# Kernel tuning notes

Measured on AMD Instinct MI355X. Metric: run time of the kernel, lower is better.

## Reference

```python
import jax, jax.numpy as jnp
import numpy as np

ALPHA = 0.5  # leaking rate, matches init_kwargs


def setup_inputs() -> dict:
    key = jax.random.key(0)
    k_x, k_i2h, k_h2h, k_ow, k_ob = jax.random.split(key, 5)
    B, T, I = 64, 256, 128
    R, O = 2048, 10
    x = jax.random.normal(k_x, (B, T, I), dtype=jnp.float32)
    # i2h_w ~ (1/sqrt(R)) * N(0,1), as in the torch module
    i2h_w = jax.random.normal(k_i2h, (I, R), dtype=jnp.float32) / np.sqrt(R)
    # h2h: random Gaussian rescaled so spectral radius ~ 0.9 (Gaussian NxN has
    # spectral radius ~ sqrt(N)); the torch code does the exact eig-based rescale
    # plus the leaky transform baked into h2h. We emulate the scale here.
    h2h = jax.random.normal(k_h2h, (R, R), dtype=jnp.float32) * (0.9 / np.sqrt(R))
    out_w = jax.random.normal(k_ow, (R, O), dtype=jnp.float32)
    out_b = jax.random.normal(k_ob, (O,), dtype=jnp.float32)
    return {"x": x, "i2h_w": i2h_w, "h2h": h2h, "out_w": out_w, "out_b": out_b}


def reference(x, i2h_w, h2h, out_w, out_b):
    # x: (B, T, I). Sequential leaky-ESN scan over T.
    B, T, I = x.shape
    R = h2h.shape[0]
    # Precompute input projections for all timesteps in one GEMM: (B, T, R)
    xin = jnp.einsum("bti,ir->btr", x, i2h_w)
    res0 = jnp.zeros((B, R), dtype=x.dtype)

    def step(res, xin_t):
        cand = jnp.tanh(xin_t + res @ h2h)
        res_new = (1.0 - ALPHA) * res + ALPHA * cand
        return res_new, res_new

    res_last, res_seq = jax.lax.scan(step, res0, jnp.swapaxes(xin, 0, 1))  # res_seq: (T, B, R)
    hiddens = jnp.swapaxes(res_seq, 0, 1)  # (B, T, R)
    # OUTPUT_TYPE.LAST_OUT -> readout of the final reservoir state
    out = res_last @ out_w + out_b  # (B, O)
    return out, hiddens
```

## Files before the change

### kernel.cpp

```cpp
#include <hip/hip_runtime.h>


typedef _Float16 f16x8 __attribute__((ext_vector_type(8)));
typedef float f32x4 __attribute__((ext_vector_type(4)));
typedef float f32x2 __attribute__((ext_vector_type(2)));

#define NB 64
#define RDIM 2048
#define TT 256
#define IDIM 128
#define NWG 128
#define NTHR 512


__global__ __launch_bounds__(256) void transpose_f32_to_f16(
    const float* __restrict__ in, _Float16* __restrict__ out, int rows, int cols) {
  __shared__ float tile[64][65];
  const int tx = threadIdx.x & 63;
  const int ty = threadIdx.x >> 6;
  const int rbase = blockIdx.y * 64;
  const int cbase = blockIdx.x * 64;
  for (int rr = ty; rr < 64; rr += 4)
    tile[rr][tx] = in[(size_t)(rbase + rr) * cols + cbase + tx];
  __syncthreads();
  for (int rr = ty; rr < 64; rr += 4)
    out[(size_t)(cbase + rr) * rows + rbase + tx] = (_Float16)tile[tx][rr];
}

__global__ __launch_bounds__(256) void convert_f32_f16(
    const float* __restrict__ in, _Float16* __restrict__ out, int n) {
  int i = blockIdx.x * 256 + threadIdx.x;
  int stride = gridDim.x * 256;
  for (; i < n; i += stride) out[i] = (_Float16)in[i];
}

__global__ __launch_bounds__(256) void init_zero(
    unsigned* __restrict__ res_words, unsigned* __restrict__ ctr_words) {
  int i = blockIdx.x * 256 + threadIdx.x;
  if (i < NB * RDIM / 2) res_words[i] = 0;
  if (i < 4096) ctr_words[i] = 0;
}


__device__ __forceinline__ f16x8 load_res16(const _Float16* p) {
  union { unsigned long long u[2]; f16x8 v; } r;
  const unsigned long long* q = (const unsigned long long*)p;
  r.u[0] = __hip_atomic_load(q, __ATOMIC_RELAXED, __HIP_MEMORY_SCOPE_SYSTEM);
  r.u[1] = __hip_atomic_load(q + 1, __ATOMIC_RELAXED, __HIP_MEMORY_SCOPE_SYSTEM);
  return r.v;
}

__device__ __forceinline__ void waitflag(const unsigned* p, unsigned tgt) {
  if (__hip_atomic_load(p, __ATOMIC_RELAXED, __HIP_MEMORY_SCOPE_SYSTEM) >= tgt) return;
  do {
    __builtin_amdgcn_s_sleep(1);
  } while (__hip_atomic_load(p, __ATOMIC_RELAXED, __HIP_MEMORY_SCOPE_SYSTEM) < tgt);
}

__device__ __forceinline__ float tanh_fast(float x) {
  float e = __expf(2.0f * x);
  return 1.0f - 2.0f * __builtin_amdgcn_rcpf(e + 1.0f);
}

__device__ __forceinline__ f32x4 MF(f16x8 a, f16x8 b, f32x4 c) {
  return __builtin_amdgcn_mfma_f32_16x16x32_f16(a, b, c, 0, 0, 0);
}


__global__ __launch_bounds__(NTHR, 2) void esn_persist(
    const _Float16* __restrict__ h2hT,
    const _Float16* __restrict__ i2hT,
    const _Float16* __restrict__ x16,
    _Float16* __restrict__ resbuf,
    float* __restrict__ pout,
    unsigned* __restrict__ ctrs,
    const float* __restrict__ out_w,
    const float* __restrict__ out_b,
    float* __restrict__ out)
{
  const int bid = blockIdx.x;
  const int rh = bid >> 6;
  const int g = bid & 63;
  const int jbase = g * 32;
  const int rbase = rh * 32;
  const int tid = threadIdx.x;
  const int wave = tid >> 6;
  const int lane = tid & 63;
  const int l15 = lane & 15;
  const int q = lane >> 4;
  const int kslice = wave * 256;

  f16x8 bfr[8][2];
#pragma unroll
  for (int kt = 0; kt < 8; ++kt)
#pragma unroll
    for (int nt = 0; nt < 2; ++nt) {
      int n_abs = jbase + nt * 16 + l15;
      bfr[kt][nt] = *(const f16x8*)(h2hT + (size_t)n_abs * RDIM + kslice + kt * 32 + q * 8);
    }
  f16x8 ib[2] = {};
  if (wave < 4) {
#pragma unroll
    for (int nt = 0; nt < 2; ++nt) {
      int n_abs = jbase + nt * 16 + l15;
      ib[nt] = *(const f16x8*)(i2hT + (size_t)n_abs * IDIM + wave * 32 + q * 8);
    }
  }

  const unsigned* fpoll = ctrs + 16 * (rh * 64 + wave * 8 + (lane & 7));

  __shared__ __align__(16) float pl[8][32][36];

  const int m = tid >> 4;
  const int c2 = (tid & 15) * 2;
  float s[2];
  s[0] = 0.f; s[1] = 0.f;

  for (int t = 0; t < TT; ++t) {
    const _Float16* resp = resbuf + (size_t)(t & 1) * (NB * RDIM);
    const unsigned tgt = (unsigned)t;

    f32x4 acc[2][2] = {};

    if (wave < 4) {
#pragma unroll
      for (int mt = 0; mt < 2; ++mt) {
        f16x8 ax = *(const f16x8*)(x16 + ((size_t)(rbase + mt * 16 + l15) * TT + t) * IDIM + wave * 32 + q * 8);
        acc[mt][0] = MF(ax, ib[0], acc[mt][0]);
        acc[mt][1] = MF(ax, ib[1], acc[mt][1]);
      }
    }

    {
      unsigned v = __hip_atomic_load(fpoll, __ATOMIC_RELAXED, __HIP_MEMORY_SCOPE_SYSTEM);
      while (!__all(v >= tgt)) {
        __builtin_amdgcn_s_sleep(1);
        v = __hip_atomic_load(fpoll, __ATOMIC_RELAXED, __HIP_MEMORY_SCOPE_SYSTEM);
      }
    }

    f16x8 A[8][2];
#pragma unroll
    for (int kt = 0; kt < 8; ++kt)
#pragma unroll
      for (int mt = 0; mt < 2; ++mt)
        A[kt][mt] = load_res16(resp + (size_t)(rbase + mt * 16 + l15) * RDIM + kslice + kt * 32 + q * 8);
#pragma unroll
    for (int kt = 0; kt < 8; ++kt)
#pragma unroll
      for (int mt = 0; mt < 2; ++mt) {
        acc[mt][0] = MF(A[kt][mt], bfr[kt][0], acc[mt][0]);
        acc[mt][1] = MF(A[kt][mt], bfr[kt][1], acc[mt][1]);
      }

#pragma unroll
    for (int mt = 0; mt < 2; ++mt)
#pragma unroll
      for (int nt = 0; nt < 2; ++nt)
#pragma unroll
        for (int r = 0; r < 4; ++r)
          pl[wave][mt * 16 + q * 4 + r][nt * 16 + l15] = acc[mt][nt][r];
    __syncthreads();

    f32x2 v = *(const f32x2*)&pl[0][m][c2];
#pragma unroll
    for (int w = 1; w < 8; ++w) v += *(const f32x2*)&pl[w][m][c2];

    union { _Float16 h[2]; unsigned u; } frag;
#pragma unroll
    for (int r = 0; r < 2; ++r) {
      s[r] = 0.5f * s[r] + 0.5f * tanh_fast(v[r]);
      frag.h[r] = (_Float16)s[r];
    }

    _Float16* resw = resbuf + (size_t)((t + 1) & 1) * (NB * RDIM);
    __hip_atomic_store((unsigned*)(resw + (size_t)(rbase + m) * RDIM + jbase + c2),
                       frag.u, __ATOMIC_RELAXED, __HIP_MEMORY_SCOPE_SYSTEM);
    __syncthreads();
    if (tid == 0)
      __hip_atomic_store(&ctrs[16 * bid], (unsigned)(t + 1), __ATOMIC_RELAXED,
                         __HIP_MEMORY_SCOPE_SYSTEM);

    f32x2 hv;
    hv[0] = s[0]; hv[1] = s[1];
    float* hid = out + 640 + ((size_t)(rbase + m) * TT + t) * RDIM + jbase + c2;
    __builtin_nontemporal_store(hv, (f32x2*)hid);
  }

  if (bid < 16) {
    if (tid == 0) {
      for (int rh2 = 0; rh2 < 2; ++rh2)
        for (int j = 0; j < 4; ++j)
          waitflag(ctrs + 16 * (rh2 * 64 + 4 * bid + j), (unsigned)TT);
    }
    __syncthreads();
    const _Float16* rlast = resbuf;
    for (int o = tid; o < 640; o += NTHR) {
      int b = o / 10, oo = o - 10 * b;
      float a = 0.f;
      const unsigned* rp = (const unsigned*)(rlast + (size_t)b * RDIM + bid * 128);
      for (int r2 = 0; r2 < 64; ++r2) {
        union { unsigned u; _Float16 h[2]; } cv;
        cv.u = __hip_atomic_load(rp + r2, __ATOMIC_RELAXED, __HIP_MEMORY_SCOPE_SYSTEM);
        a += (float)cv.h[0] * out_w[(size_t)(bid * 128 + 2 * r2) * 10 + oo];
        a += (float)cv.h[1] * out_w[(size_t)(bid * 128 + 2 * r2 + 1) * 10 + oo];
      }
      __hip_atomic_store(&pout[bid * 640 + o], a, __ATOMIC_RELAXED, __HIP_MEMORY_SCOPE_SYSTEM);
    }
    __syncthreads();
    if (tid == 0)
      __hip_atomic_fetch_add(&ctrs[2048], 1u, __ATOMIC_RELAXED, __HIP_MEMORY_SCOPE_SYSTEM);
    if (bid == 0) {
      if (tid == 0) {
        while (__hip_atomic_load(&ctrs[2048], __ATOMIC_RELAXED, __HIP_MEMORY_SCOPE_SYSTEM) < 16u)
          __builtin_amdgcn_s_sleep(1);
      }
      __syncthreads();
      for (int o = tid; o < 640; o += NTHR) {
        float a = out_b[o % 10];
        for (int kk = 0; kk < 16; ++kk)
          a += __hip_atomic_load(&pout[kk * 640 + o], __ATOMIC_RELAXED, __HIP_MEMORY_SCOPE_SYSTEM);
        out[o] = a;
      }
    }
  }
}


extern "C" void kernel_launch(void* const* d_in, const int* in_sizes, int n_in,
                              void* d_out, int out_size, void* d_ws, size_t ws_size,
                              hipStream_t stream) {
  const float* x     = (const float*)d_in[0];
  const float* i2h_w = (const float*)d_in[1];
  const float* h2h   = (const float*)d_in[2];
  const float* out_w = (const float*)d_in[3];
  const float* out_b = (const float*)d_in[4];
  float* out = (float*)d_out;

  unsigned char* ws = (unsigned char*)d_ws;
  _Float16* h2hT   = (_Float16*)(ws + 0);
  _Float16* i2hT   = (_Float16*)(ws + 8388608);
  _Float16* x16    = (_Float16*)(ws + 8912896);
  _Float16* resbuf = (_Float16*)(ws + 13107200);
  float*    pout   = (float*)   (ws + 13631488);
  unsigned* ctrs   = (unsigned*)(ws + 13672448);

  transpose_f32_to_f16<<<dim3(32, 32), dim3(256), 0, stream>>>(h2h, h2hT, 2048, 2048);
  transpose_f32_to_f16<<<dim3(32, 2), dim3(256), 0, stream>>>(i2h_w, i2hT, 128, 2048);
  convert_f32_f16<<<dim3(512), dim3(256), 0, stream>>>(x, x16, NB * TT * IDIM);
  init_zero<<<dim3(256), dim3(256), 0, stream>>>((unsigned*)resbuf, ctrs);
  esn_persist<<<dim3(NWG), dim3(NTHR), 0, stream>>>(h2hT, i2hT, x16, resbuf, pout,
                                                    ctrs, out_w, out_b, out);
}
```

Baseline: 2.311 ms.

## Stage h2h B-fragments in LDS and reduce wave partials with LDS atomics

Moves the per-wave h2h weight fragments out of registers into shared memory and reloads them from LDS each timestep, which frees VGPRs. The separate per-wave partial-sum planes and their 8-way reduction are replaced by LDS atomicAdd into a single 32x36 tile, which is zeroed after it is read. It also adds an explicit vmcnt wait and a scheduling barrier before the MFMA loop. The trade is extra LDS traffic on every step and atomic contention between waves, in exchange for lower register pressure and a smaller reduction footprint.

```diff
diff --git a/kernel.cpp b/kernel.cpp
--- a/kernel.cpp
+++ b/kernel.cpp
@@ -90,13 +90,16 @@
   const int q = lane >> 4;
   const int kslice = wave * 256;
 
-  f16x8 bfr[8][2];
+  __shared__ __align__(16) _Float16 blds[8 * 16 * 64 * 8];
+  __shared__ __align__(16) float pl[32][36];
+
 #pragma unroll
   for (int kt = 0; kt < 8; ++kt)
 #pragma unroll
     for (int nt = 0; nt < 2; ++nt) {
       int n_abs = jbase + nt * 16 + l15;
-      bfr[kt][nt] = *(const f16x8*)(h2hT + (size_t)n_abs * RDIM + kslice + kt * 32 + q * 8);
+      f16x8 bv = *(const f16x8*)(h2hT + (size_t)n_abs * RDIM + kslice + kt * 32 + q * 8);
+      *(f16x8*)(blds + (size_t)((wave * 16 + kt * 2 + nt) * 64 + lane) * 8) = bv;
     }
   f16x8 ib[2] = {};
   if (wave < 4) {
@@ -106,15 +109,17 @@
       ib[nt] = *(const f16x8*)(i2hT + (size_t)n_abs * IDIM + wave * 32 + q * 8);
     }
   }
+  for (int i = tid; i < 32 * 36; i += NTHR) ((float*)pl)[i] = 0.f;
+  __syncthreads();
 
   const unsigned* fpoll = ctrs + 16 * (rh * 64 + wave * 8 + (lane & 7));
-
-  __shared__ __align__(16) float pl[8][32][36];
 
   const int m = tid >> 4;
   const int c2 = (tid & 15) * 2;
   float s[2];
   s[0] = 0.f; s[1] = 0.f;
+
+  const _Float16* bw = blds + (size_t)wave * 16 * 64 * 8;
 
   for (int t = 0; t < TT; ++t) {
     const _Float16* resp = resbuf + (size_t)(t & 1) * (NB * RDIM);
@@ -145,13 +150,18 @@
 #pragma unroll
       for (int mt = 0; mt < 2; ++mt)
         A[kt][mt] = load_res16(resp + (size_t)(rbase + mt * 16 + l15) * RDIM + kslice + kt * 32 + q * 8);
-#pragma unroll
-    for (int kt = 0; kt < 8; ++kt)
-#pragma unroll
-      for (int mt = 0; mt < 2; ++mt) {
-        acc[mt][0] = MF(A[kt][mt], bfr[kt][0], acc[mt][0]);
-        acc[mt][1] = MF(A[kt][mt], bfr[kt][1], acc[mt][1]);
-      }
+    asm volatile("s_waitcnt vmcnt(0)" ::: "memory");
+    __builtin_amdgcn_sched_barrier(0);
+
+#pragma unroll
+    for (int kt = 0; kt < 8; ++kt) {
+      f16x8 b0 = *(const f16x8*)(bw + (size_t)((kt * 2 + 0) * 64 + lane) * 8);
+      f16x8 b1 = *(const f16x8*)(bw + (size_t)((kt * 2 + 1) * 64 + lane) * 8);
+      acc[0][0] = MF(A[kt][0], b0, acc[0][0]);
+      acc[1][0] = MF(A[kt][1], b0, acc[1][0]);
+      acc[0][1] = MF(A[kt][0], b1, acc[0][1]);
+      acc[1][1] = MF(A[kt][1], b1, acc[1][1]);
+    }
 
 #pragma unroll
     for (int mt = 0; mt < 2; ++mt)
@@ -159,19 +169,19 @@
       for (int nt = 0; nt < 2; ++nt)
 #pragma unroll
         for (int r = 0; r < 4; ++r)
-          pl[wave][mt * 16 + q * 4 + r][nt * 16 + l15] = acc[mt][nt][r];
-    __syncthreads();
-
-    f32x2 v = *(const f32x2*)&pl[0][m][c2];
-#pragma unroll
-    for (int w = 1; w < 8; ++w) v += *(const f32x2*)&pl[w][m][c2];
+          atomicAdd(&pl[mt * 16 + q * 4 + r][nt * 16 + l15], acc[mt][nt][r]);
+    __syncthreads();
+
+    float v0 = pl[m][c2];
+    float v1 = pl[m][c2 + 1];
+    pl[m][c2] = 0.f;
+    pl[m][c2 + 1] = 0.f;
 
     union { _Float16 h[2]; unsigned u; } frag;
-#pragma unroll
-    for (int r = 0; r < 2; ++r) {
-      s[r] = 0.5f * s[r] + 0.5f * tanh_fast(v[r]);
-      frag.h[r] = (_Float16)s[r];
-    }
+    s[0] = 0.5f * s[0] + 0.5f * tanh_fast(v0);
+    s[1] = 0.5f * s[1] + 0.5f * tanh_fast(v1);
+    frag.h[0] = (_Float16)s[0];
+    frag.h[1] = (_Float16)s[1];
 
     _Float16* resw = resbuf + (size_t)((t + 1) & 1) * (NB * RDIM);
     __hip_atomic_store((unsigned*)(resw + (size_t)(rbase + m) * RDIM + jbase + c2),
```

Result: slower. 3.748 ms (+62.2%).
